# Kernel tuning notes

Hardware: AMD Instinct MI355X
Metric: run time of the kernel (lower is better)

Reference implementation:

```python
import jax, jax.numpy as jnp
import numpy as np

D_MODEL = 1024
NUM_HEADS = 16
HEAD_DIM = D_MODEL // NUM_HEADS


def setup_inputs() -> dict:
    key = jax.random.key(0)
    k_x, k_wqkv, k_bqkv, k_wo, k_bo = jax.random.split(key, 5)
    x = jax.random.normal(k_x, (2, 2048, D_MODEL), dtype=jnp.float32)
    s = 1.0 / np.sqrt(D_MODEL)
    W_qkv = jax.random.uniform(k_wqkv, (D_MODEL, 3 * D_MODEL), jnp.float32, -s, s)
    b_qkv = jax.random.uniform(k_bqkv, (3 * D_MODEL,), jnp.float32, -s, s)
    W_o = jax.random.uniform(k_wo, (D_MODEL, D_MODEL), jnp.float32, -s, s)
    b_o = jax.random.uniform(k_bo, (D_MODEL,), jnp.float32, -s, s)
    return {"x": x, "W_qkv": W_qkv, "b_qkv": b_qkv, "W_o": W_o, "b_o": b_o}


def reference(x, W_qkv, b_qkv, W_o, b_o):
    B, S, D = x.shape
    # fused QKV projection: [B,S,3D]
    qkv = jnp.einsum('bsd,de->bse', x, W_qkv) + b_qkv
    # [B,S,H,3*hd] -> [B,H,S,3*hd]
    qkv = qkv.reshape(B, S, NUM_HEADS, 3 * HEAD_DIM).transpose(0, 2, 1, 3)
    q, k, v = jnp.split(qkv, 3, axis=-1)  # each [B,H,S,hd]
    scale = 1.0 / jnp.sqrt(jnp.asarray(HEAD_DIM, dtype=x.dtype))
    scores = jnp.einsum('bhqd,bhkd->bhqk', q, k) * scale  # [B,H,S,S]
    attn = jax.nn.softmax(scores, axis=-1)
    values = jnp.einsum('bhqk,bhkd->bhqd', attn, v)  # [B,H,S,hd]
    values = values.transpose(0, 2, 1, 3).reshape(B, S, D)
    out = jnp.einsum('bsd,de->bse', values, W_o) + b_o
    return out
```

## Files before the change

### kernel.cpp

```cpp
#include <hip/hip_runtime.h>
#include <stdint.h>
#include <stddef.h>

typedef _Float16 f16;
typedef _Float16 f16x8 __attribute__((ext_vector_type(8)));
typedef _Float16 f16x4 __attribute__((ext_vector_type(4)));
typedef float    f32x2 __attribute__((ext_vector_type(2)));
typedef float    f32x4 __attribute__((ext_vector_type(4)));
typedef float    f32x16 __attribute__((ext_vector_type(16)));
typedef int      i32x4 __attribute__((ext_vector_type(4)));
typedef int      i32x2 __attribute__((ext_vector_type(2)));

#define S_LEN 2048
#define DM    1024
#define NH    16
#define HD    64
#define NTOK  4096
#define NQKV  3072
#define QSCALE 0.18033688011112042f

#if __has_builtin(__builtin_amdgcn_exp2f)
#define EXP2(x) __builtin_amdgcn_exp2f(x)
#else
#define EXP2(x) __expf((x) * 0.69314718055994531f)
#endif

__device__ __forceinline__ void gl_lds16(const void* g, void* l) {
  __builtin_amdgcn_global_load_lds(
      (const __attribute__((address_space(1))) void*)g,
      (__attribute__((address_space(3))) void*)l, 16, 0, 0);
}

__device__ __forceinline__ void pl32_swap(int& a, int& b) {
#if __has_builtin(__builtin_amdgcn_permlane32_swap)
  i32x2 r = __builtin_amdgcn_permlane32_swap(a, b, false, false);
  a = r.x; b = r.y;
#else
  asm volatile("v_permlane32_swap_b32 %0, %1" : "+v"(a), "+v"(b));
#endif
}

__device__ __forceinline__ float swap_half(float x, int hi) {
  int a = __builtin_bit_cast(int, x);
  int b = a;
  pl32_swap(a, b);
  return __builtin_bit_cast(float, hi ? a : b);
}

__device__ __forceinline__ int pkrtz(float a, float b) {
  auto h = __builtin_amdgcn_cvt_pkrtz(a, b);
  return __builtin_bit_cast(int, h);
}

__device__ __forceinline__ f16x8 mk_frag(int a, int b, int c, int d) {
  i32x4 v = {a, b, c, d};
  return __builtin_bit_cast(f16x8, v);
}

__device__ __forceinline__ f32x2 pk2(const f32x16& v, int i) {
  f32x2 r = {v[2*i], v[2*i+1]};
  return r;
}

__global__ __launch_bounds__(256) void cvt_f16_kernel(const float* __restrict__ in,
                                                      f16* __restrict__ out, int n) {
  int i = (blockIdx.x * 256 + threadIdx.x) * 8;
  if (i >= n) return;
  float4 a = *(const float4*)(in + i);
  float4 b = *(const float4*)(in + i + 4);
  f16x8 v = {(f16)a.x,(f16)a.y,(f16)a.z,(f16)a.w,(f16)b.x,(f16)b.y,(f16)b.z,(f16)b.w};
  *(f16x8*)(out + i) = v;
}

__global__ __launch_bounds__(256) void cvt_tr_kernel(const float* __restrict__ in,
                                                     f16* __restrict__ out, int R, int C) {
  __shared__ float t[32][33];
  int c0 = blockIdx.x * 32, r0 = blockIdx.y * 32;
  int tx = threadIdx.x, ty = threadIdx.y;
  #pragma unroll
  for (int i = 0; i < 4; ++i)
    t[ty + i*8][tx] = in[(size_t)(r0 + ty + i*8) * C + c0 + tx];
  __syncthreads();
  #pragma unroll
  for (int i = 0; i < 4; ++i)
    out[(size_t)(c0 + ty + i*8) * R + r0 + tx] = (f16)t[tx][ty + i*8];
}

template<int EPI>
__global__ __launch_bounds__(256) void gemm128_kernel(
    const f16* __restrict__ A, const f16* __restrict__ Bt,
    const float* __restrict__ bias,
    f16* __restrict__ qb, f16* __restrict__ kb, f16* __restrict__ vtb,
    float* __restrict__ out)
{
  __shared__ f16 As[128*64];
  __shared__ f16 Bs[128*64];
  const int tid = threadIdx.x;
  const int wid = tid >> 6, lane = tid & 63;
  const int g = lane >> 4, r = lane & 15;
  const int flat = blockIdx.x;
  const int xcd = flat & 7, idx = flat >> 3;
  const int m0 = (xcd * 4 + (idx & 3)) * 128;
  const int n0 = (idx >> 2) * 128;
  const int wm = (wid >> 1) * 64, wn = (wid & 1) * 64;

  f32x4 acc[4][4] = {};
  int soff[4];
  #pragma unroll
  for (int c = 0; c < 4; ++c) {
    int ca = tid + c*256, pr = ca >> 3, pc = ca & 7, lc = pc ^ (pr & 7);
    soff[c] = pr * DM + lc * 8;
  }
  const f16* Ab = A  + (size_t)m0 * DM;
  const f16* Bb = Bt + (size_t)n0 * DM;

  for (int kt = 0; kt < 16; ++kt) {
    __syncthreads();
    #pragma unroll
    for (int c = 0; c < 4; ++c) {
      gl_lds16(Ab + kt*64 + soff[c], (char*)As + c*4096 + tid*16);
      gl_lds16(Bb + kt*64 + soff[c], (char*)Bs + c*4096 + tid*16);
    }
    __syncthreads();
    #pragma unroll
    for (int kk = 0; kk < 2; ++kk) {
      f16x8 a[4], b[4];
      #pragma unroll
      for (int mt = 0; mt < 4; ++mt) {
        int rl = wm + mt*16 + r;
        a[mt] = *(const f16x8*)(As + rl*64 + (((kk*4 + g) ^ (rl & 7)) * 8));
      }
      #pragma unroll
      for (int nt = 0; nt < 4; ++nt) {
        int cl = wn + nt*16 + r;
        b[nt] = *(const f16x8*)(Bs + cl*64 + (((kk*4 + g) ^ (cl & 7)) * 8));
      }
      #pragma unroll
      for (int mt = 0; mt < 4; ++mt)
        #pragma unroll
        for (int nt = 0; nt < 4; ++nt)
          acc[mt][nt] = __builtin_amdgcn_mfma_f32_16x16x32_f16(a[mt], b[nt], acc[mt][nt], 0, 0, 0);
    }
  }

  if (EPI == 0) {
    #pragma unroll
    for (int mt = 0; mt < 4; ++mt) {
      int row0 = m0 + wm + mt*16 + g*4;
      int b_ = row0 >> 11, s0 = row0 & 2047;
      #pragma unroll
      for (int nt = 0; nt < 4; ++nt) {
        int col = n0 + wn + nt*16 + r;
        float bv = bias[col];
        int h = col / 192;
        int cc = col - h*192;
        int which = cc >> 6, d = cc & 63;
        size_t bh = (size_t)(b_*NH + h);
        if (which == 2) {
          f16x4 v;
          #pragma unroll
          for (int i = 0; i < 4; ++i) v[i] = (f16)(acc[mt][nt][i] + bv);
          *(f16x4*)(vtb + (bh*HD + d)*S_LEN + s0) = v;
        } else if (which == 0) {
          #pragma unroll
          for (int i = 0; i < 4; ++i)
            qb[(bh*S_LEN + s0 + i)*HD + d] = (f16)((acc[mt][nt][i] + bv) * QSCALE);
        } else {
          #pragma unroll
          for (int i = 0; i < 4; ++i)
            kb[(bh*S_LEN + s0 + i)*HD + d] = (f16)(acc[mt][nt][i] + bv);
        }
      }
    }
  } else {
    #pragma unroll
    for (int mt = 0; mt < 4; ++mt) {
      int row0 = m0 + wm + mt*16 + g*4;
      #pragma unroll
      for (int nt = 0; nt < 4; ++nt) {
        int col = n0 + wn + nt*16 + r;
        float bv = bias[col];
        #pragma unroll
        for (int i = 0; i < 4; ++i)
          out[(size_t)(row0 + i)*DM + col] = acc[mt][nt][i] + bv;
      }
    }
  }
}

__global__ __launch_bounds__(256) void attn_kernel(
    const f16* __restrict__ qb, const f16* __restrict__ kb,
    const f16* __restrict__ vtb, f16* __restrict__ values)
{
  __shared__ __align__(16) char smem[33280];

  const int tid = threadIdx.x;
  const int wid = tid >> 6, lane = tid & 63;
  const int ql = lane & 31, hi = lane >> 5;
  const int flat = blockIdx.x;
  const int xcd = flat & 7, idx = flat >> 3;
  const int bh = xcd * 4 + (idx & 3);
  const int q0 = (idx >> 2) * 128 + wid * 32;
  const f16* qh = qb  + (size_t)bh * S_LEN * HD;
  const f16* kh = kb  + (size_t)bh * S_LEN * HD;
  const f16* vh = vtb + (size_t)bh * HD * S_LEN;

  int koff[2], voff[2];
  #pragma unroll
  for (int c = 0; c < 2; ++c) {
    int ca = tid + c*256, pr = ca >> 4, pc = ca & 15, lc = pc ^ (pr & 15);
    int row2 = pr*2 + (lc >> 3), e8 = (lc & 7) * 8;
    koff[c] = row2 * HD + e8;
    voff[c] = row2 * S_LEN + e8;
  }

  f16x8 qf[4];
  #pragma unroll
  for (int dk = 0; dk < 4; ++dk)
    qf[dk] = *(const f16x8*)(qh + (size_t)(q0 + ql)*HD + dk*16 + hi*8);

  const int r0b = (ql >> 1) << 8;
  const int xv  = (ql >> 1) & 15;
  const int hb  = ((ql & 1) << 3) | hi;

  f32x2 lacc = {0.f, 0.f};
  f32x16 o0 = {}, o1 = {};
  f32x16 sX0, sX1, sY0, sY1;

  #define STAGE_K(kt_, buf_) do {                                          \
    const f16* ks_ = kh + (size_t)((kt_)*64) * HD;                         \
    char* kd_ = smem + (buf_)*8192;                                        \
    gl_lds16(ks_ + koff[0], kd_ + tid*16);                                 \
    gl_lds16(ks_ + koff[1], kd_ + 4096 + tid*16);                          \
  } while (0)
  #define STAGE_V(kt_, buf_) do {                                          \
    const f16* vs_ = vh + (kt_)*64;                                        \
    char* vd_ = smem + 16384 + (buf_)*8192;                                \
    gl_lds16(vs_ + voff[0], vd_ + tid*16);                                 \
    gl_lds16(vs_ + voff[1], vd_ + 4096 + tid*16);                          \
  } while (0)

  #define QK_H(S_, KsC_, base_) do {                                       \
    S_ = (f32x16){};                                                       \
    _Pragma("unroll")                                                      \
    for (int dk = 0; dk < 4; ++dk) {                                       \
      int off = r0b + (((hb | (dk << 1)) ^ xv) << 4);                      \
      f16x8 kf = *(const f16x8*)((KsC_) + (base_) + off);                  \
      S_ = __builtin_amdgcn_mfma_f32_32x32x16_f16(kf, qf[dk], S_, 0, 0, 0);\
    }                                                                      \
  } while (0)

  #define EXP_H(S_, PFA_, PFB_) do {                                       \
    _Pragma("unroll")                                                      \
    for (int i = 0; i < 16; ++i) S_[i] = EXP2(S_[i]);                      \
    f32x2 sm[4];                                                           \
    _Pragma("unroll")                                                      \
    for (int i = 0; i < 4; ++i) sm[i] = pk2(S_, i) + pk2(S_, i + 4);       \
    sm[0] += sm[1]; sm[2] += sm[3]; lacc += sm[0] + sm[2];                 \
    int a = pkrtz(S_[0], S_[1]), b = pkrtz(S_[2], S_[3]);                  \
    int c = pkrtz(S_[4], S_[5]), d = pkrtz(S_[6], S_[7]);                  \
    pl32_swap(a, c); pl32_swap(b, d);                                      \
    PFA_ = mk_frag(a, b, c, d);                                            \
    a = pkrtz(S_[8],  S_[9]);  b = pkrtz(S_[10], S_[11]);                  \
    c = pkrtz(S_[12], S_[13]); d = pkrtz(S_[14], S_[15]);                  \
    pl32_swap(a, c); pl32_swap(b, d);                                      \
    PFB_ = mk_frag(a, b, c, d);                                            \
  } while (0)

  #define PVQ(buf_) do {                                                   \
    const char* VsC = smem + 16384 + (buf_)*8192;                          \
    __builtin_amdgcn_s_setprio(1);                                         \
    _Pragma("unroll")                                                      \
    for (int w = 0; w < 4; ++w) {                                          \
      int off = r0b + (((hb | (w << 1)) ^ xv) << 4);                       \
      f16x8 vf0 = *(const f16x8*)(VsC + off);                              \
      f16x8 vf1 = *(const f16x8*)(VsC + 4096 + off);                       \
      o0 = __builtin_amdgcn_mfma_f32_32x32x16_f16(pf[w], vf0, o0, 0, 0, 0);\
      o1 = __builtin_amdgcn_mfma_f32_32x32x16_f16(pf[w], vf1, o1, 0, 0, 0);\
    }                                                                      \
    __builtin_amdgcn_s_setprio(0);                                         \
  } while (0)

  #define BODY(SA0_, SA1_, SB0_, SB1_, kt_, cur_) do {                     \
    const char* KsN = smem + ((cur_) ^ 1)*8192;                            \
    STAGE_V((kt_) + 1, (cur_) ^ 1);                                        \
    if ((kt_) < 30) STAGE_K((kt_) + 2, (cur_));                            \
    QK_H(SB0_, KsN, 0);                                                    \
    EXP_H(SA0_, pf[0], pf[1]);                                             \
    QK_H(SB1_, KsN, 4096);                                                 \
    EXP_H(SA1_, pf[2], pf[3]);                                             \
    PVQ(cur_);                                                             \
    __syncthreads();                                                       \
  } while (0)

  STAGE_K(0, 0); STAGE_V(0, 0); STAGE_K(1, 1);
  __syncthreads();
  f16x8 pf[4];
  QK_H(sX0, smem, 0);
  QK_H(sX1, smem, 4096);
  __syncthreads();

  for (int kt2 = 0; kt2 < 30; kt2 += 2) {
    BODY(sX0, sX1, sY0, sY1, kt2,     0);
    BODY(sY0, sY1, sX0, sX1, kt2 + 1, 1);
  }
  BODY(sX0, sX1, sY0, sY1, 30, 0);
  EXP_H(sY0, pf[0], pf[1]);
  EXP_H(sY1, pf[2], pf[3]);
  PVQ(1);

  #undef STAGE_K
  #undef STAGE_V
  #undef QK_H
  #undef EXP_H
  #undef PVQ
  #undef BODY

  float l_run = lacc.x + lacc.y;
  l_run += swap_half(l_run, hi);
  float inv = 1.0f / l_run;
  float* cb = (float*)(smem + 32768) + wid*32;
  cb[ql] = inv;
  __syncthreads();
  f32x4 vinv[4];
  #pragma unroll
  for (int t = 0; t < 4; ++t)
    vinv[t] = *(const f32x4*)(cb + hi*4 + t*8);

  const int b_ = bh >> 4, h = bh & 15;
  #pragma unroll
  for (int t = 0; t < 4; ++t)
    #pragma unroll
    for (int i = 0; i < 4; ++i) {
      int qrow = q0 + 4*hi + 8*t + i;
      size_t base = (size_t)(b_*S_LEN + qrow) * DM + h*HD + ql;
      values[base]      = (f16)(o0[t*4+i] * vinv[t][i]);
      values[base + 32] = (f16)(o1[t*4+i] * vinv[t][i]);
    }
}

extern "C" void kernel_launch(void* const* d_in, const int* in_sizes, int n_in,
                              void* d_out, int out_size, void* d_ws, size_t ws_size,
                              hipStream_t stream) {
  (void)in_sizes; (void)n_in; (void)out_size; (void)ws_size;
  const float* x    = (const float*)d_in[0];
  const float* Wqkv = (const float*)d_in[1];
  const float* bqkv = (const float*)d_in[2];
  const float* Wo   = (const float*)d_in[3];
  const float* bo   = (const float*)d_in[4];
  float* out = (float*)d_out;

  char* ws = (char*)d_ws;
  f16* x_h    = (f16*)(ws);
  f16* Wqkv_t = (f16*)(ws + ( 8ull<<20));
  f16* Wo_t   = (f16*)(ws + (14ull<<20));
  f16* qbuf   = (f16*)(ws + (16ull<<20));
  f16* kbuf   = (f16*)(ws + (24ull<<20));
  f16* vtbuf  = (f16*)(ws + (32ull<<20));
  f16* vals   = (f16*)(ws + (40ull<<20));

  cvt_f16_kernel<<<dim3(NTOK*DM/8/256), dim3(256), 0, stream>>>(x, x_h, NTOK*DM);
  cvt_tr_kernel<<<dim3(NQKV/32, DM/32), dim3(32, 8), 0, stream>>>(Wqkv, Wqkv_t, DM, NQKV);
  cvt_tr_kernel<<<dim3(DM/32, DM/32),  dim3(32, 8), 0, stream>>>(Wo, Wo_t, DM, DM);

  gemm128_kernel<0><<<dim3(768), dim3(256), 0, stream>>>(
      x_h, Wqkv_t, bqkv, qbuf, kbuf, vtbuf, nullptr);

  attn_kernel<<<dim3(512), dim3(256), 0, stream>>>(qbuf, kbuf, vtbuf, vals);

  gemm128_kernel<1><<<dim3(256), dim3(256), 0, stream>>>(
      vals, Wo_t, bo, nullptr, nullptr, nullptr, out);
}
```

Before: 126.7 us.

## Deepen K prefetch to four LDS buffers and shrink GEMM K-tile to 32

The attention kernel now keeps four K tiles in LDS and prefetches K three iterations ahead. The full __syncthreads at the end of each step becomes an explicit vmcnt wait plus s_barrier, so later loads can stay in flight while earlier ones are consumed. The GEMM kernel halves its K-tile from 64 to 32, with a new swizzle, which cuts LDS use but doubles the number of barrier-separated iterations. The larger attention LDS footprint may lower occupancy, and the manual vmcnt count, including the clamped duplicate loads of the last K tile, must exactly match the issued loads to stay correct.

Measured after the change: 118.2 us. -6.7%, faster.

```diff
diff --git a/kernel.cpp b/kernel.cpp
--- a/kernel.cpp
+++ b/kernel.cpp
@@ -93,8 +93,8 @@
     f16* __restrict__ qb, f16* __restrict__ kb, f16* __restrict__ vtb,
     float* __restrict__ out)
 {
-  __shared__ f16 As[128*64];
-  __shared__ f16 Bs[128*64];
+  __shared__ f16 As[128*32];
+  __shared__ f16 Bs[128*32];
   const int tid = threadIdx.x;
   const int wid = tid >> 6, lane = tid & 63;
   const int g = lane >> 4, r = lane & 15;
@@ -105,42 +105,36 @@
   const int wm = (wid >> 1) * 64, wn = (wid & 1) * 64;
 
   f32x4 acc[4][4] = {};
-  int soff[4];
-  #pragma unroll
-  for (int c = 0; c < 4; ++c) {
-    int ca = tid + c*256, pr = ca >> 3, pc = ca & 7, lc = pc ^ (pr & 7);
-    soff[c] = pr * DM + lc * 8;
-  }
-  const f16* Ab = A  + (size_t)m0 * DM;
-  const f16* Bb = Bt + (size_t)n0 * DM;
-
-  for (int kt = 0; kt < 16; ++kt) {
+  const int srow = tid >> 2;
+  const int sch  = tid & 3;
+
+  for (int kt = 0; kt < DM/32; ++kt) {
+    const int k0 = kt * 32;
     __syncthreads();
     #pragma unroll
-    for (int c = 0; c < 4; ++c) {
-      gl_lds16(Ab + kt*64 + soff[c], (char*)As + c*4096 + tid*16);
-      gl_lds16(Bb + kt*64 + soff[c], (char*)Bs + c*4096 + tid*16);
+    for (int c = 0; c < 2; ++c) {
+      int row = c*64 + srow;
+      int sw = (sch ^ ((row >> 1) & 3)) * 8;
+      gl_lds16(A  + (size_t)(m0 + row) * DM + k0 + sw, (char*)As + c*4096 + tid*16);
+      gl_lds16(Bt + (size_t)(n0 + row) * DM + k0 + sw, (char*)Bs + c*4096 + tid*16);
     }
     __syncthreads();
-    #pragma unroll
-    for (int kk = 0; kk < 2; ++kk) {
-      f16x8 a[4], b[4];
+    f16x8 a[4], b[4];
+    #pragma unroll
+    for (int mt = 0; mt < 4; ++mt) {
+      int rl = wm + mt*16 + r;
+      a[mt] = *(const f16x8*)(As + rl*32 + ((g ^ ((rl >> 1) & 3)) * 8));
+    }
+    #pragma unroll
+    for (int nt = 0; nt < 4; ++nt) {
+      int cl = wn + nt*16 + r;
+      b[nt] = *(const f16x8*)(Bs + cl*32 + ((g ^ ((cl >> 1) & 3)) * 8));
+    }
+    #pragma unroll
+    for (int mt = 0; mt < 4; ++mt)
       #pragma unroll
-      for (int mt = 0; mt < 4; ++mt) {
-        int rl = wm + mt*16 + r;
-        a[mt] = *(const f16x8*)(As + rl*64 + (((kk*4 + g) ^ (rl & 7)) * 8));
-      }
-      #pragma unroll
-      for (int nt = 0; nt < 4; ++nt) {
-        int cl = wn + nt*16 + r;
-        b[nt] = *(const f16x8*)(Bs + cl*64 + (((kk*4 + g) ^ (cl & 7)) * 8));
-      }
-      #pragma unroll
-      for (int mt = 0; mt < 4; ++mt)
-        #pragma unroll
-        for (int nt = 0; nt < 4; ++nt)
-          acc[mt][nt] = __builtin_amdgcn_mfma_f32_16x16x32_f16(a[mt], b[nt], acc[mt][nt], 0, 0, 0);
-    }
+      for (int nt = 0; nt < 4; ++nt)
+        acc[mt][nt] = __builtin_amdgcn_mfma_f32_16x16x32_f16(a[mt], b[nt], acc[mt][nt], 0, 0, 0);
   }
 
   if (EPI == 0) {
@@ -192,7 +186,7 @@
     const f16* __restrict__ qb, const f16* __restrict__ kb,
     const f16* __restrict__ vtb, f16* __restrict__ values)
 {
-  __shared__ __align__(16) char smem[33280];
+  __shared__ __align__(16) char smem[49664];
 
   const int tid = threadIdx.x;
   const int wid = tid >> 6, lane = tid & 63;
@@ -235,7 +229,7 @@
   } while (0)
   #define STAGE_V(kt_, buf_) do {                                          \
     const f16* vs_ = vh + (kt_)*64;                                        \
-    char* vd_ = smem + 16384 + (buf_)*8192;                                \
+    char* vd_ = smem + 16384*2 + (buf_)*8192;                              \
     gl_lds16(vs_ + voff[0], vd_ + tid*16);                                 \
     gl_lds16(vs_ + voff[1], vd_ + 4096 + tid*16);                          \
   } while (0)
@@ -268,7 +262,7 @@
   } while (0)
 
   #define PVQ(buf_) do {                                                   \
-    const char* VsC = smem + 16384 + (buf_)*8192;                          \
+    const char* VsC = smem + 16384*2 + (buf_)*8192;                        \
     __builtin_amdgcn_s_setprio(1);                                         \
     _Pragma("unroll")                                                      \
     for (int w = 0; w < 4; ++w) {                                          \
@@ -281,19 +275,22 @@
     __builtin_amdgcn_s_setprio(0);                                         \
   } while (0)
 
-  #define BODY(SA0_, SA1_, SB0_, SB1_, kt_, cur_) do {                     \
-    const char* KsN = smem + ((cur_) ^ 1)*8192;                            \
-    STAGE_V((kt_) + 1, (cur_) ^ 1);                                        \
-    if ((kt_) < 30) STAGE_K((kt_) + 2, (cur_));                            \
+  #define BODY(SA0_, SA1_, SB0_, SB1_, kt_) do {                           \
+    const char* KsN = smem + (((kt_) + 1) & 3)*8192;                       \
+    const int kst_ = ((kt_) + 4 > 31) ? 31 : ((kt_) + 4);                  \
+    STAGE_V((kt_) + 1, ((kt_) + 1) & 1);                                   \
+    STAGE_K(kst_, (kt_) & 3);                                              \
     QK_H(SB0_, KsN, 0);                                                    \
     EXP_H(SA0_, pf[0], pf[1]);                                             \
     QK_H(SB1_, KsN, 4096);                                                 \
     EXP_H(SA1_, pf[2], pf[3]);                                             \
-    PVQ(cur_);                                                             \
-    __syncthreads();                                                       \
-  } while (0)
-
-  STAGE_K(0, 0); STAGE_V(0, 0); STAGE_K(1, 1);
+    PVQ((kt_) & 1);                                                        \
+    asm volatile("s_waitcnt vmcnt(2)" ::: "memory");                       \
+    __builtin_amdgcn_s_barrier();                                          \
+    __builtin_amdgcn_sched_barrier(0);                                     \
+  } while (0)
+
+  STAGE_K(0, 0); STAGE_V(0, 0); STAGE_K(1, 1); STAGE_K(2, 2); STAGE_K(3, 3);
   __syncthreads();
   f16x8 pf[4];
   QK_H(sX0, smem, 0);
@@ -301,10 +298,10 @@
   __syncthreads();
 
   for (int kt2 = 0; kt2 < 30; kt2 += 2) {
-    BODY(sX0, sX1, sY0, sY1, kt2,     0);
-    BODY(sY0, sY1, sX0, sX1, kt2 + 1, 1);
+    BODY(sX0, sX1, sY0, sY1, kt2);
+    BODY(sY0, sY1, sX0, sX1, kt2 + 1);
   }
-  BODY(sX0, sX1, sY0, sY1, 30, 0);
+  BODY(sX0, sX1, sY0, sY1, 30);
   EXP_H(sY0, pf[0], pf[1]);
   EXP_H(sY1, pf[2], pf[3]);
   PVQ(1);
@@ -319,7 +316,8 @@
   float l_run = lacc.x + lacc.y;
   l_run += swap_half(l_run, hi);
   float inv = 1.0f / l_run;
-  float* cb = (float*)(smem + 32768) + wid*32;
+  float* cb = (float*)(smem + 49152) + wid*32;
+  __syncthreads();
   cb[ql] = inv;
   __syncthreads();
   f32x4 vinv[4];
```
